# Kernel optimization log

Hardware: AMD Instinct MI355X
Metric: run time of the kernel (lower is better)

## Reference

```python
import jax, jax.numpy as jnp
import numpy as np

N_NODES = 50000
N_EDGES = 640000
D_IN = 128
D_HID = 128


def gcn_conv(x, W, b, src, dst, num_nodes):
    """PyG GCNConv: add self-loops, symmetric normalization, aggregate at target.

    src/dst already include self-loops. x: [N, F_in], W: [F_in, F_out].
    """
    h = x @ W  # [N, F_out] dense transform first (PyG default order)
    ones = jnp.ones(src.shape[0], dtype=h.dtype)
    deg = jax.ops.segment_sum(ones, dst, num_segments=num_nodes)  # in-degree w/ self loops
    dinv = jnp.where(deg > 0, jax.lax.rsqrt(deg), 0.0)
    norm = dinv[src] * dinv[dst]  # [E+N]
    msgs = h[src] * norm[:, None]  # gather + edge-wise scale
    out = jax.ops.segment_sum(msgs, dst, num_segments=num_nodes)  # scatter-add at target
    return out + b


def setup_inputs() -> dict:
    key = jax.random.key(0)
    k1, k2, k3, k4 = jax.random.split(key, 4)
    x = jax.random.normal(k1, (N_NODES, D_IN), dtype=jnp.float32)
    edge_index = jax.random.randint(k2, (2, N_EDGES), 0, N_NODES, dtype=jnp.int64)
    # Glorot-ish init for weights
    W1 = jax.random.normal(k3, (D_IN, D_HID), dtype=jnp.float32) * (1.0 / np.sqrt(D_IN))
    b1 = jnp.zeros((D_HID,), dtype=jnp.float32)
    W2 = jax.random.normal(k4, (D_HID, D_HID), dtype=jnp.float32) * (1.0 / np.sqrt(D_HID))
    b2 = jnp.zeros((D_HID,), dtype=jnp.float32)
    return {"x": x, "edge_index": edge_index, "W1": W1, "b1": b1, "W2": W2, "b2": b2}


def reference(x, edge_index, W1, b1, W2, b2):
    num_nodes = x.shape[0]
    loop = jnp.arange(num_nodes, dtype=edge_index.dtype)
    src = jnp.concatenate([edge_index[0], loop])  # add self-loops once; shared by both convs
    dst = jnp.concatenate([edge_index[1], loop])
    h = jax.nn.relu(gcn_conv(x, W1, b1, src, dst, num_nodes))
    out = gcn_conv(h, W2, b2, src, dst, num_nodes)
    return out
```

## Files before the change

### kernel.cpp

```cpp
#include <hip/hip_runtime.h>

#define NN 50000
#define NE 640000
#define DF 128
#define BM 64
#define BSH 7
#define BWD 128
#define NBKT ((NN + BWD - 1) / BWD)
#define BSTRIDE 4096
#define CPAD 16
#define EPB 8192
#define TPB 512
#define MROWS 50048

typedef __attribute__((ext_vector_type(8))) short short8;
typedef __attribute__((ext_vector_type(4))) float f32x4;

__device__ inline unsigned bf16rne(float f) {
  unsigned u = __float_as_uint(f);
  return (u + 0x7fff + ((u >> 16) & 1)) >> 16;
}
__device__ inline float bflo(unsigned u) { return __uint_as_float(u << 16); }
__device__ inline float bfhi(unsigned u) { return __uint_as_float(u & 0xffff0000u); }
__device__ inline float bfs(unsigned short h) { return __uint_as_float(((unsigned)h) << 16); }


__global__ __launch_bounds__(512) void k_zb(int* __restrict__ gfill) {
  for (int i = threadIdx.x; i < NBKT * CPAD; i += 512) gfill[i] = 0;
}

__global__ __launch_bounds__(512) void k_bscatter(const int* __restrict__ ei, int* __restrict__ gfill,
                                                  unsigned* __restrict__ pairs) {
  __shared__ int cnt[NBKT];
  __shared__ int cur[NBKT];
  __shared__ int gbase[NBKT];
  __shared__ int scan[TPB];
  __shared__ unsigned stage[EPB];
  int t = threadIdx.x;
  int e0 = blockIdx.x * EPB;

  for (int i = t; i < NBKT; i += TPB) cnt[i] = 0;
  __syncthreads();

  unsigned pk[16];
  int bk[16];
#pragma unroll
  for (int i = 0; i < 16; ++i) {
    int e = e0 + i * TPB + t;
    if (e < NE) {
      int s = ei[e], d = ei[NE + e];
      bk[i] = d >> BSH;
      pk[i] = (unsigned)s | ((unsigned)(d & (BWD - 1)) << 16);
      atomicAdd(&cnt[bk[i]], 1);
    } else {
      bk[i] = -1;
    }
  }
  __syncthreads();

  int v = (t < NBKT) ? cnt[t] : 0;
  scan[t] = v;
  __syncthreads();
  for (int d = 1; d < TPB; d <<= 1) {
    int x = (t >= d) ? scan[t - d] : 0;
    __syncthreads();
    scan[t] += x;
    __syncthreads();
  }
  if (t < NBKT) {
    int start = scan[t] - v;
    cnt[t] = start;
    cur[t] = start;
    gbase[t] = (v > 0) ? atomicAdd(&gfill[t * CPAD], v) : 0;
  }
  __syncthreads();

#pragma unroll
  for (int i = 0; i < 16; ++i) {
    if (bk[i] >= 0) {
      int pos = atomicAdd(&cur[bk[i]], 1);
      stage[pos] = pk[i];
    }
  }
  __syncthreads();

  int wv = t >> 6, ln = t & 63;
  for (int b = wv; b < NBKT; b += 8) {
    int start = cnt[b];
    int end = cur[b];
    int gb = gbase[b];
    unsigned* pb = pairs + (size_t)b * BSTRIDE;
    for (int i = start + ln; i < end; i += 64) {
      int go = gb + (i - start);
      if (go < BSTRIDE) pb[go] = stage[i];
    }
  }
}

__global__ __launch_bounds__(512) void k_bscan(const int* __restrict__ gfill, int* __restrict__ boff) {
  __shared__ int s[512];
  int t = threadIdx.x;
  int v = (t < NBKT) ? min(gfill[t * CPAD], BSTRIDE) : 0;
  s[t] = v;
  __syncthreads();
  for (int d = 1; d < 512; d <<= 1) {
    int x = (t >= d) ? s[t - d] : 0;
    __syncthreads();
    s[t] += x;
    __syncthreads();
  }
  if (t < NBKT) boff[t] = s[t] - v;
  if (t == 511) boff[NBKT] = s[511];
}

__global__ __launch_bounds__(256) void k_build(const unsigned* __restrict__ pairs,
                                               const int* __restrict__ boff,
                                               int* __restrict__ off, float* __restrict__ dinv,
                                               unsigned short* __restrict__ ssrc) {
  __shared__ int lcnt[BWD];
  __shared__ int lfill[BWD];
  __shared__ int s[BWD];
  __shared__ unsigned short stage[BSTRIDE];
  int b = blockIdx.x, t = threadIdx.x;
  int e0 = boff[b];
  int n = boff[b + 1] - e0;
  const unsigned* pb = pairs + (size_t)b * BSTRIDE;

  if (t < BWD) lcnt[t] = 0;
  __syncthreads();
  for (int i = t; i < n; i += 256) atomicAdd(&lcnt[pb[i] >> 16], 1);
  __syncthreads();

  int cnt = (t < BWD) ? lcnt[t] : 0;
  if (t < BWD) s[t] = cnt;
  __syncthreads();
  for (int d = 1; d < BWD; d <<= 1) {
    int x = (t >= d && t < BWD) ? s[t - d] : 0;
    __syncthreads();
    if (t < BWD) s[t] += x;
    __syncthreads();
  }
  int node = b * BWD + t;
  if (t < BWD) {
    int ex = s[t] - cnt;
    lfill[t] = ex;
    if (node < NN) {
      off[node] = e0 + ex;
      dinv[node] = rsqrtf((float)(cnt + 1));
    }
    if (node == NN - 1) off[NN] = NE;
  }
  __syncthreads();

  for (int i = t; i < n; i += 256) {
    unsigned p = pb[i];
    int pos = atomicAdd(&lfill[p >> 16], 1);
    stage[pos] = (unsigned short)(p & 0xffffu);
  }
  __syncthreads();
  for (int i = t; i < n; i += 256) ssrc[e0 + i] = stage[i];
}


__global__ __launch_bounds__(256) void k_wpack(const float* __restrict__ W1, const float* __restrict__ W2,
                                               uint4* __restrict__ whf, uint4* __restrict__ wlf) {
  int idx = blockIdx.x * 256 + threadIdx.x;
  if (idx >= 4096) return;
  int m = idx >> 11;
  int r = idx & 2047;
  int ct = r >> 8, kc = (r >> 6) & 3, l = r & 63;
  const float* W = m ? W2 : W1;
  unsigned hi[8], lo[8];
#pragma unroll
  for (int j = 0; j < 8; ++j) {
    int k = kc * 32 + (l >> 4) * 8 + j;
    int c = ct * 16 + (l & 15);
    float w = W[k * DF + c];
    unsigned h = bf16rne(w);
    hi[j] = h;
    lo[j] = bf16rne(w - bflo(h));
  }
  uint4 H, L;
  H.x = hi[0] | (hi[1] << 16); H.y = hi[2] | (hi[3] << 16);
  H.z = hi[4] | (hi[5] << 16); H.w = hi[6] | (hi[7] << 16);
  L.x = lo[0] | (lo[1] << 16); L.y = lo[2] | (lo[3] << 16);
  L.z = lo[4] | (lo[5] << 16); L.w = lo[6] | (lo[7] << 16);
  whf[idx] = H;
  wlf[idx] = L;
}


template <int ABF16>
__global__ __launch_bounds__(256) void k_gemm(const void* __restrict__ Av,
                                              const uint4* __restrict__ whf,
                                              const uint4* __restrict__ wlf,
                                              const float* __restrict__ dinv,
                                              unsigned* __restrict__ C) {
  __shared__ float Ep[4][16][132];
  int t = threadIdx.x, w = t >> 6, l = t & 63;
  int brow = blockIdx.x * BM + w * 16;
  int ra = brow + (l & 15);
  bool inb = ra < NN;

  short8 Ah[4], Al[4];
#pragma unroll
  for (int kc = 0; kc < 4; ++kc) {
    if (ABF16) {
      uint4 u = make_uint4(0, 0, 0, 0);
      if (inb) u = ((const uint4*)Av)[(size_t)ra * 16 + kc * 4 + (l >> 4)];
      Ah[kc] = *(short8*)&u;
      Al[kc] = short8{0, 0, 0, 0, 0, 0, 0, 0};
    } else {
      float f[8] = {0.f, 0.f, 0.f, 0.f, 0.f, 0.f, 0.f, 0.f};
      if (inb) {
        const float* A = (const float*)Av + (size_t)ra * DF + kc * 32 + (l >> 4) * 8;
        float4 p = *(const float4*)A;
        float4 q = *(const float4*)(A + 4);
        f[0] = p.x; f[1] = p.y; f[2] = p.z; f[3] = p.w;
        f[4] = q.x; f[5] = q.y; f[6] = q.z; f[7] = q.w;
      }
      unsigned hh[8], ll[8];
#pragma unroll
      for (int j = 0; j < 8; ++j) {
        hh[j] = bf16rne(f[j]);
        ll[j] = bf16rne(f[j] - bflo(hh[j]));
      }
      uint4 H, L;
      H.x = hh[0] | (hh[1] << 16); H.y = hh[2] | (hh[3] << 16);
      H.z = hh[4] | (hh[5] << 16); H.w = hh[6] | (hh[7] << 16);
      L.x = ll[0] | (ll[1] << 16); L.y = ll[2] | (ll[3] << 16);
      L.z = ll[4] | (ll[5] << 16); L.w = ll[6] | (ll[7] << 16);
      Ah[kc] = *(short8*)&H;
      Al[kc] = *(short8*)&L;
    }
  }

  f32x4 acc[8];
#pragma unroll
  for (int ct = 0; ct < 8; ++ct) acc[ct] = f32x4{0.f, 0.f, 0.f, 0.f};

#pragma unroll
  for (int kc = 0; kc < 4; ++kc) {
#pragma unroll
    for (int ct = 0; ct < 8; ++ct) {
      int fi = (ct * 4 + kc) * 64 + l;
      uint4 wh4 = whf[fi];
      uint4 wl4 = wlf[fi];
      short8 wh = *(short8*)&wh4;
      short8 wl = *(short8*)&wl4;
      acc[ct] = __builtin_amdgcn_mfma_f32_16x16x32_bf16(Ah[kc], wh, acc[ct], 0, 0, 0);
      acc[ct] = __builtin_amdgcn_mfma_f32_16x16x32_bf16(Ah[kc], wl, acc[ct], 0, 0, 0);
      if (!ABF16)
        acc[ct] = __builtin_amdgcn_mfma_f32_16x16x32_bf16(Al[kc], wh, acc[ct], 0, 0, 0);
    }
  }

#pragma unroll
  for (int ct = 0; ct < 8; ++ct) {
#pragma unroll
    for (int reg = 0; reg < 4; ++reg)
      Ep[w][(l >> 4) * 4 + reg][ct * 16 + (l & 15)] = acc[ct][reg];
  }

  int r16 = l >> 2, cc = (l & 3) * 32;
  int R = blockIdx.x * BM + w * 16 + r16;
  float sc = (R < NN) ? dinv[R] : 0.f;
  unsigned ub[16];
#pragma unroll
  for (int i = 0; i < 16; ++i) {
    float f0 = Ep[w][r16][cc + 2 * i] * sc;
    float f1 = Ep[w][r16][cc + 2 * i + 1] * sc;
    ub[i] = bf16rne(f0) | (bf16rne(f1) << 16);
  }
  uint4* co = (uint4*)(C + (size_t)R * 64 + (cc >> 1));
  co[0] = make_uint4(ub[0], ub[1], ub[2], ub[3]);
  co[1] = make_uint4(ub[4], ub[5], ub[6], ub[7]);
  co[2] = make_uint4(ub[8], ub[9], ub[10], ub[11]);
  co[3] = make_uint4(ub[12], ub[13], ub[14], ub[15]);
}


template <int OUTBF16>
__global__ __launch_bounds__(256) void k_agg(const unsigned* __restrict__ h, const float* __restrict__ dinv,
                                             const int* __restrict__ off, const unsigned short* __restrict__ ssrc,
                                             const float* __restrict__ bias, void* __restrict__ out) {
  int gw = (blockIdx.x * 256 + threadIdx.x) >> 6;
  int lane = threadIdx.x & 63;
  if (gw >= NN) return;

  int c = lane & 15;
  int q = lane >> 4;

  float acc[8];
  {
    uint4 u = *((const uint4*)(h + (size_t)gw * 64) + c);
    float m = (q == 0) ? 1.f : 0.f;
    acc[0] = bflo(u.x) * m; acc[1] = bfhi(u.x) * m;
    acc[2] = bflo(u.y) * m; acc[3] = bfhi(u.y) * m;
    acc[4] = bflo(u.z) * m; acc[5] = bfhi(u.z) * m;
    acc[6] = bflo(u.w) * m; acc[7] = bfhi(u.w) * m;
  }

  int e = off[gw], e1 = off[gw + 1];
  for (int e0 = e; e0 < e1; e0 += 8) {
    int ea = e0 + q;
    int eb = e0 + 4 + q;
    int sa = (ea < e1) ? (int)ssrc[ea] : NN;
    int sb = (eb < e1) ? (int)ssrc[eb] : NN;
    uint4 ua = *((const uint4*)(h + (size_t)sa * 64) + c);
    uint4 ub = *((const uint4*)(h + (size_t)sb * 64) + c);
    acc[0] += bflo(ua.x); acc[1] += bfhi(ua.x);
    acc[2] += bflo(ua.y); acc[3] += bfhi(ua.y);
    acc[4] += bflo(ua.z); acc[5] += bfhi(ua.z);
    acc[6] += bflo(ua.w); acc[7] += bfhi(ua.w);
    acc[0] += bflo(ub.x); acc[1] += bfhi(ub.x);
    acc[2] += bflo(ub.y); acc[3] += bfhi(ub.y);
    acc[4] += bflo(ub.z); acc[5] += bfhi(ub.z);
    acc[6] += bflo(ub.w); acc[7] += bfhi(ub.w);
  }

#pragma unroll
  for (int j = 0; j < 8; ++j) {
    acc[j] += __shfl_xor(acc[j], 16);
    acc[j] += __shfl_xor(acc[j], 32);
  }

  if (q < 2) {
    float di = dinv[gw];
    int col0 = c * 8 + q * 4;
    float4 b4 = *(const float4*)(bias + col0);
    float o0 = fmaf(acc[q * 4 + 0], di, b4.x);
    float o1 = fmaf(acc[q * 4 + 1], di, b4.y);
    float o2 = fmaf(acc[q * 4 + 2], di, b4.z);
    float o3 = fmaf(acc[q * 4 + 3], di, b4.w);
    if (OUTBF16) {
      o0 = fmaxf(o0, 0.f); o1 = fmaxf(o1, 0.f);
      o2 = fmaxf(o2, 0.f); o3 = fmaxf(o3, 0.f);
      uint2 p;
      p.x = bf16rne(o0) | (bf16rne(o1) << 16);
      p.y = bf16rne(o2) | (bf16rne(o3) << 16);
      *(uint2*)((unsigned*)out + (size_t)gw * (DF / 2) + c * 4 + q * 2) = p;
    } else {
      float4 o = make_float4(o0, o1, o2, o3);
      *(float4*)((float*)out + (size_t)gw * DF + col0) = o;
    }
  }
}


extern "C" void kernel_launch(void* const* d_in, const int* in_sizes, int n_in,
                              void* d_out, int out_size, void* d_ws, size_t ws_size,
                              hipStream_t stream) {
  const float* x  = (const float*)d_in[0];
  const int*   ei = (const int*)d_in[1];
  const float* W1 = (const float*)d_in[2];
  const float* b1 = (const float*)d_in[3];
  const float* W2 = (const float*)d_in[4];
  const float* b2 = (const float*)d_in[5];
  float* out = (float*)d_out;

  char* ws = (char*)d_ws;
  unsigned* hT    = (unsigned*)ws; ws += (size_t)MROWS * (DF / 2) * 4;
  unsigned* act   = (unsigned*)ws; ws += (size_t)MROWS * (DF / 2) * 4;
  unsigned* pairs = (unsigned*)ws; ws += (size_t)NBKT * BSTRIDE * 4;
  uint4* whf = (uint4*)ws;  ws += (size_t)4096 * 16;
  uint4* wlf = (uint4*)ws;  ws += (size_t)4096 * 16;
  int*   off  = (int*)ws;   ws += (size_t)(NN + 1) * 4;
  int*   gfill= (int*)ws;   ws += (size_t)NBKT * CPAD * 4;
  int*   boff = (int*)ws;   ws += (size_t)(NBKT + 1) * 4;
  float* dinv = (float*)ws; ws += (size_t)NN * 4;
  unsigned short* ssrc = (unsigned short*)ws; ws += ((size_t)NE + 16) * 2;

  const int GGRID = MROWS / BM;

  k_zb<<<1, 512, 0, stream>>>(gfill);
  k_bscatter<<<(NE + EPB - 1) / EPB, TPB, 0, stream>>>(ei, gfill, pairs);
  k_bscan<<<1, 512, 0, stream>>>(gfill, boff);
  k_wpack<<<16, 256, 0, stream>>>(W1, W2, whf, wlf);
  k_build<<<NBKT, 256, 0, stream>>>(pairs, boff, off, dinv, ssrc);

  k_gemm<0><<<GGRID, 256, 0, stream>>>(x, whf, wlf, dinv, hT);
  k_agg<1><<<(NN * 64 + 255) / 256, 256, 0, stream>>>(hT, dinv, off, ssrc, b1, act);
  k_gemm<1><<<GGRID, 256, 0, stream>>>(act, whf + 2048, wlf + 2048, dinv, hT);
  k_agg<0><<<(NN * 64 + 255) / 256, 256, 0, stream>>>(hT, dinv, off, ssrc, b2, out);
}
```

Measured before the change: 138.8 us.

## Fuse graph build with first GEMM and layer-1 aggregation with second GEMM

Cuts the pipeline from nine launches to five. Weight packing and bucket-counter zeroing share one kernel. Edge bucket-scatter and the first dense transform run as disjoint block ranges of a single launch, so they can overlap. The separate bucket scan is folded into the build kernel, where each block reduces the earlier bucket counts itself. The layer-1 aggregation now writes its 64-row tile of activations into shared memory and feeds the second MFMA GEMM in the same kernel, and the dinv[src] scaling moves into the gather instead of the first GEMM epilogue. Buckets are widened to 256 nodes, which halves the bucket count. The costs are serialised aggregation of 16 rows per wave pass inside each fused block, lower occupancy, and redundant prefix sums across build blocks.

```diff
diff --git a/kernel.cpp b/kernel.cpp
--- a/kernel.cpp
+++ b/kernel.cpp
@@ -3,15 +3,15 @@
 #define NN 50000
 #define NE 640000
 #define DF 128
-#define BM 64
-#define BSH 7
-#define BWD 128
-#define NBKT ((NN + BWD - 1) / BWD)
-#define BSTRIDE 4096
+#define BSH 8
+#define BWD 256
+#define NBKT 196
+#define BSTRIDE 8192
 #define CPAD 16
 #define EPB 8192
-#define TPB 512
+#define NSB ((NE + EPB - 1) / EPB)
 #define MROWS 50048
+#define GG 782
 
 typedef __attribute__((ext_vector_type(8))) short short8;
 typedef __attribute__((ext_vector_type(4))) float f32x4;
@@ -22,150 +22,16 @@
 }
 __device__ inline float bflo(unsigned u) { return __uint_as_float(u << 16); }
 __device__ inline float bfhi(unsigned u) { return __uint_as_float(u & 0xffff0000u); }
-__device__ inline float bfs(unsigned short h) { return __uint_as_float(((unsigned)h) << 16); }
-
-
-__global__ __launch_bounds__(512) void k_zb(int* __restrict__ gfill) {
-  for (int i = threadIdx.x; i < NBKT * CPAD; i += 512) gfill[i] = 0;
-}
-
-__global__ __launch_bounds__(512) void k_bscatter(const int* __restrict__ ei, int* __restrict__ gfill,
-                                                  unsigned* __restrict__ pairs) {
-  __shared__ int cnt[NBKT];
-  __shared__ int cur[NBKT];
-  __shared__ int gbase[NBKT];
-  __shared__ int scan[TPB];
-  __shared__ unsigned stage[EPB];
-  int t = threadIdx.x;
-  int e0 = blockIdx.x * EPB;
-
-  for (int i = t; i < NBKT; i += TPB) cnt[i] = 0;
-  __syncthreads();
-
-  unsigned pk[16];
-  int bk[16];
-#pragma unroll
-  for (int i = 0; i < 16; ++i) {
-    int e = e0 + i * TPB + t;
-    if (e < NE) {
-      int s = ei[e], d = ei[NE + e];
-      bk[i] = d >> BSH;
-      pk[i] = (unsigned)s | ((unsigned)(d & (BWD - 1)) << 16);
-      atomicAdd(&cnt[bk[i]], 1);
-    } else {
-      bk[i] = -1;
-    }
-  }
-  __syncthreads();
-
-  int v = (t < NBKT) ? cnt[t] : 0;
-  scan[t] = v;
-  __syncthreads();
-  for (int d = 1; d < TPB; d <<= 1) {
-    int x = (t >= d) ? scan[t - d] : 0;
-    __syncthreads();
-    scan[t] += x;
-    __syncthreads();
-  }
-  if (t < NBKT) {
-    int start = scan[t] - v;
-    cnt[t] = start;
-    cur[t] = start;
-    gbase[t] = (v > 0) ? atomicAdd(&gfill[t * CPAD], v) : 0;
-  }
-  __syncthreads();
-
-#pragma unroll
-  for (int i = 0; i < 16; ++i) {
-    if (bk[i] >= 0) {
-      int pos = atomicAdd(&cur[bk[i]], 1);
-      stage[pos] = pk[i];
-    }
-  }
-  __syncthreads();
-
-  int wv = t >> 6, ln = t & 63;
-  for (int b = wv; b < NBKT; b += 8) {
-    int start = cnt[b];
-    int end = cur[b];
-    int gb = gbase[b];
-    unsigned* pb = pairs + (size_t)b * BSTRIDE;
-    for (int i = start + ln; i < end; i += 64) {
-      int go = gb + (i - start);
-      if (go < BSTRIDE) pb[go] = stage[i];
-    }
-  }
-}
-
-__global__ __launch_bounds__(512) void k_bscan(const int* __restrict__ gfill, int* __restrict__ boff) {
-  __shared__ int s[512];
-  int t = threadIdx.x;
-  int v = (t < NBKT) ? min(gfill[t * CPAD], BSTRIDE) : 0;
-  s[t] = v;
-  __syncthreads();
-  for (int d = 1; d < 512; d <<= 1) {
-    int x = (t >= d) ? s[t - d] : 0;
-    __syncthreads();
-    s[t] += x;
-    __syncthreads();
-  }
-  if (t < NBKT) boff[t] = s[t] - v;
-  if (t == 511) boff[NBKT] = s[511];
-}
-
-__global__ __launch_bounds__(256) void k_build(const unsigned* __restrict__ pairs,
-                                               const int* __restrict__ boff,
-                                               int* __restrict__ off, float* __restrict__ dinv,
-                                               unsigned short* __restrict__ ssrc) {
-  __shared__ int lcnt[BWD];
-  __shared__ int lfill[BWD];
-  __shared__ int s[BWD];
-  __shared__ unsigned short stage[BSTRIDE];
-  int b = blockIdx.x, t = threadIdx.x;
-  int e0 = boff[b];
-  int n = boff[b + 1] - e0;
-  const unsigned* pb = pairs + (size_t)b * BSTRIDE;
-
-  if (t < BWD) lcnt[t] = 0;
-  __syncthreads();
-  for (int i = t; i < n; i += 256) atomicAdd(&lcnt[pb[i] >> 16], 1);
-  __syncthreads();
-
-  int cnt = (t < BWD) ? lcnt[t] : 0;
-  if (t < BWD) s[t] = cnt;
-  __syncthreads();
-  for (int d = 1; d < BWD; d <<= 1) {
-    int x = (t >= d && t < BWD) ? s[t - d] : 0;
-    __syncthreads();
-    if (t < BWD) s[t] += x;
-    __syncthreads();
-  }
-  int node = b * BWD + t;
-  if (t < BWD) {
-    int ex = s[t] - cnt;
-    lfill[t] = ex;
-    if (node < NN) {
-      off[node] = e0 + ex;
-      dinv[node] = rsqrtf((float)(cnt + 1));
-    }
-    if (node == NN - 1) off[NN] = NE;
-  }
-  __syncthreads();
-
-  for (int i = t; i < n; i += 256) {
-    unsigned p = pb[i];
-    int pos = atomicAdd(&lfill[p >> 16], 1);
-    stage[pos] = (unsigned short)(p & 0xffffu);
-  }
-  __syncthreads();
-  for (int i = t; i < n; i += 256) ssrc[e0 + i] = stage[i];
-}
-
-
-__global__ __launch_bounds__(256) void k_wpack(const float* __restrict__ W1, const float* __restrict__ W2,
-                                               uint4* __restrict__ whf, uint4* __restrict__ wlf) {
+
+
+__global__ __launch_bounds__(256) void k_wz(const float* __restrict__ W1, const float* __restrict__ W2,
+                                            uint4* __restrict__ whf, uint4* __restrict__ wlf,
+                                            int* __restrict__ gfill) {
+  if (blockIdx.x == 16) {
+    for (int i = threadIdx.x; i < NBKT * CPAD; i += 256) gfill[i] = 0;
+    return;
+  }
   int idx = blockIdx.x * 256 + threadIdx.x;
-  if (idx >= 4096) return;
   int m = idx >> 11;
   int r = idx & 2047;
   int ct = r >> 8, kc = (r >> 6) & 3, l = r & 63;
@@ -190,34 +56,96 @@
 }
 
 
-template <int ABF16>
-__global__ __launch_bounds__(256) void k_gemm(const void* __restrict__ Av,
-                                              const uint4* __restrict__ whf,
-                                              const uint4* __restrict__ wlf,
-                                              const float* __restrict__ dinv,
-                                              unsigned* __restrict__ C) {
-  __shared__ float Ep[4][16][132];
-  int t = threadIdx.x, w = t >> 6, l = t & 63;
-  int brow = blockIdx.x * BM + w * 16;
-  int ra = brow + (l & 15);
-  bool inb = ra < NN;
-
-  short8 Ah[4], Al[4];
-#pragma unroll
-  for (int kc = 0; kc < 4; ++kc) {
-    if (ABF16) {
-      uint4 u = make_uint4(0, 0, 0, 0);
-      if (inb) u = ((const uint4*)Av)[(size_t)ra * 16 + kc * 4 + (l >> 4)];
-      Ah[kc] = *(short8*)&u;
-      Al[kc] = short8{0, 0, 0, 0, 0, 0, 0, 0};
-    } else {
+struct ScatSh {
+  int cnt[NBKT], cur[NBKT], gbase[NBKT];
+  int scan[256];
+  unsigned stage[EPB];
+};
+struct GemmSh { float Ep[4][16][132]; };
+union SgSh { ScatSh s; GemmSh g; };
+
+__global__ __launch_bounds__(256) void k_sg(const int* __restrict__ ei, int* __restrict__ gfill,
+                                            unsigned* __restrict__ pairs,
+                                            const float* __restrict__ X,
+                                            const uint4* __restrict__ whf, const uint4* __restrict__ wlf,
+                                            unsigned* __restrict__ hA) {
+  __shared__ SgSh sh;
+  int t = threadIdx.x;
+
+  if (blockIdx.x < NSB) {
+    int e0 = blockIdx.x * EPB;
+    for (int i = t; i < NBKT; i += 256) sh.s.cnt[i] = 0;
+    __syncthreads();
+
+    unsigned pk[32];
+    int bk[32];
+#pragma unroll
+    for (int i = 0; i < 32; ++i) {
+      int e = e0 + i * 256 + t;
+      if (e < NE) {
+        int s = ei[e], d = ei[NE + e];
+        bk[i] = d >> BSH;
+        pk[i] = (unsigned)s | ((unsigned)(d & (BWD - 1)) << 16);
+        atomicAdd(&sh.s.cnt[bk[i]], 1);
+      } else {
+        bk[i] = -1;
+      }
+    }
+    __syncthreads();
+
+    int v = (t < NBKT) ? sh.s.cnt[t] : 0;
+    sh.s.scan[t] = v;
+    __syncthreads();
+    for (int d = 1; d < 256; d <<= 1) {
+      int x2 = (t >= d) ? sh.s.scan[t - d] : 0;
+      __syncthreads();
+      sh.s.scan[t] += x2;
+      __syncthreads();
+    }
+    if (t < NBKT) {
+      int start = sh.s.scan[t] - v;
+      sh.s.cnt[t] = start;
+      sh.s.cur[t] = start;
+      sh.s.gbase[t] = (v > 0) ? atomicAdd(&gfill[t * CPAD], v) : 0;
+    }
+    __syncthreads();
+
+#pragma unroll
+    for (int i = 0; i < 32; ++i) {
+      if (bk[i] >= 0) {
+        int pos = atomicAdd(&sh.s.cur[bk[i]], 1);
+        sh.s.stage[pos] = pk[i];
+      }
+    }
+    __syncthreads();
+
+    int wv = t >> 6, ln = t & 63;
+    for (int b = wv; b < NBKT; b += 4) {
+      int start = sh.s.cnt[b];
+      int end = sh.s.cur[b];
+      int gb = sh.s.gbase[b];
+      unsigned* pb = pairs + (size_t)b * BSTRIDE;
+      for (int i = start + ln; i < end; i += 64) {
+        int go = gb + (i - start);
+        if (go < BSTRIDE) pb[go] = sh.s.stage[i];
+      }
+    }
+  } else {
+    int w = t >> 6, l = t & 63;
+    int brow = (blockIdx.x - NSB) * 64 + w * 16;
+    int ra = brow + (l & 15);
+    bool inb = ra < NN;
+
+    short8 Ah[4], Al[4];
+#pragma unroll
+    for (int kc = 0; kc < 4; ++kc) {
       float f[8] = {0.f, 0.f, 0.f, 0.f, 0.f, 0.f, 0.f, 0.f};
       if (inb) {
-        const float* A = (const float*)Av + (size_t)ra * DF + kc * 32 + (l >> 4) * 8;
+        const float* A = X + (size_t)ra * DF + kc * 32 + (l >> 4) * 8;
         float4 p = *(const float4*)A;
-        float4 q = *(const float4*)(A + 4);
+        float4 qq = *(const float4*)(A + 4);
         f[0] = p.x; f[1] = p.y; f[2] = p.z; f[3] = p.w;
-        f[4] = q.x; f[5] = q.y; f[6] = q.z; f[7] = q.w;
+        f[4] = qq.x; f[5] = qq.y; f[6] = qq.z; f[7] = qq.w;
       }
       unsigned hh[8], ll[8];
 #pragma unroll
@@ -233,11 +161,189 @@
       Ah[kc] = *(short8*)&H;
       Al[kc] = *(short8*)&L;
     }
-  }
-
-  f32x4 acc[8];
-#pragma unroll
-  for (int ct = 0; ct < 8; ++ct) acc[ct] = f32x4{0.f, 0.f, 0.f, 0.f};
+
+    f32x4 acc[8];
+#pragma unroll
+    for (int ct = 0; ct < 8; ++ct) acc[ct] = f32x4{0.f, 0.f, 0.f, 0.f};
+
+#pragma unroll
+    for (int kc = 0; kc < 4; ++kc) {
+#pragma unroll
+      for (int ct = 0; ct < 8; ++ct) {
+        int fi = (ct * 4 + kc) * 64 + l;
+        uint4 wh4 = whf[fi];
+        uint4 wl4 = wlf[fi];
+        short8 wh = *(short8*)&wh4;
+        short8 wl = *(short8*)&wl4;
+        acc[ct] = __builtin_amdgcn_mfma_f32_16x16x32_bf16(Ah[kc], wh, acc[ct], 0, 0, 0);
+        acc[ct] = __builtin_amdgcn_mfma_f32_16x16x32_bf16(Ah[kc], wl, acc[ct], 0, 0, 0);
+        acc[ct] = __builtin_amdgcn_mfma_f32_16x16x32_bf16(Al[kc], wh, acc[ct], 0, 0, 0);
+      }
+    }
+
+#pragma unroll
+    for (int ct = 0; ct < 8; ++ct)
+#pragma unroll
+      for (int reg = 0; reg < 4; ++reg)
+        sh.g.Ep[w][(l >> 4) * 4 + reg][ct * 16 + (l & 15)] = acc[ct][reg];
+
+    int r16 = l >> 2, cc = (l & 3) * 32;
+    int R = (blockIdx.x - NSB) * 64 + w * 16 + r16;
+    float sc = (R < NN) ? 1.f : 0.f;
+    unsigned ub[16];
+#pragma unroll
+    for (int i = 0; i < 16; ++i) {
+      float f0 = sh.g.Ep[w][r16][cc + 2 * i] * sc;
+      float f1 = sh.g.Ep[w][r16][cc + 2 * i + 1] * sc;
+      ub[i] = bf16rne(f0) | (bf16rne(f1) << 16);
+    }
+    uint4* co = (uint4*)(hA + (size_t)R * 64 + (cc >> 1));
+    co[0] = make_uint4(ub[0], ub[1], ub[2], ub[3]);
+    co[1] = make_uint4(ub[4], ub[5], ub[6], ub[7]);
+    co[2] = make_uint4(ub[8], ub[9], ub[10], ub[11]);
+    co[3] = make_uint4(ub[12], ub[13], ub[14], ub[15]);
+  }
+}
+
+
+__global__ __launch_bounds__(256) void k_build(const unsigned* __restrict__ pairs,
+                                               const int* __restrict__ gfill,
+                                               int* __restrict__ off, float* __restrict__ dinv,
+                                               unsigned short* __restrict__ ssrc) {
+  __shared__ int lcnt[BWD];
+  __shared__ int lfill[BWD];
+  __shared__ int s[BWD];
+  __shared__ int red[256];
+  __shared__ unsigned short stage[BSTRIDE];
+  int b = blockIdx.x, t = threadIdx.x;
+
+  int part = 0;
+  for (int j = t; j < b; j += 256) part += min(gfill[j * CPAD], BSTRIDE);
+  red[t] = part;
+  __syncthreads();
+  for (int d = 128; d > 0; d >>= 1) {
+    if (t < d) red[t] += red[t + d];
+    __syncthreads();
+  }
+  int e0 = red[0];
+  int n = min(gfill[b * CPAD], BSTRIDE);
+  const unsigned* pb = pairs + (size_t)b * BSTRIDE;
+
+  lcnt[t] = 0;
+  __syncthreads();
+  for (int i = t; i < n; i += 256) atomicAdd(&lcnt[pb[i] >> 16], 1);
+  __syncthreads();
+
+  int cnt = lcnt[t];
+  s[t] = cnt;
+  __syncthreads();
+  for (int d = 1; d < 256; d <<= 1) {
+    int x = (t >= d) ? s[t - d] : 0;
+    __syncthreads();
+    s[t] += x;
+    __syncthreads();
+  }
+  int node = b * BWD + t;
+  int ex = s[t] - cnt;
+  lfill[t] = ex;
+  if (node < NN) {
+    off[node] = e0 + ex;
+    dinv[node] = rsqrtf((float)(cnt + 1));
+  }
+  if (node == NN - 1) off[NN] = NE;
+  __syncthreads();
+
+  for (int i = t; i < n; i += 256) {
+    unsigned p = pb[i];
+    int pos = atomicAdd(&lfill[p >> 16], 1);
+    stage[pos] = (unsigned short)(p & 0xffffu);
+  }
+  __syncthreads();
+  for (int i = t; i < n; i += 256) ssrc[e0 + i] = stage[i];
+}
+
+
+__global__ __launch_bounds__(256) void k_aggemm(const unsigned* __restrict__ hA,
+                                                const float* __restrict__ dinv,
+                                                const int* __restrict__ off,
+                                                const unsigned short* __restrict__ ssrc,
+                                                const float* __restrict__ b1,
+                                                const uint4* __restrict__ whf,
+                                                const uint4* __restrict__ wlf,
+                                                unsigned* __restrict__ hB) {
+  __shared__ unsigned actS[64][68];
+  __shared__ float Ep[4][16][132];
+  int t = threadIdx.x, w = t >> 6, l = t & 63;
+  int brow = blockIdx.x * 64;
+  int c = l & 15, q = l >> 4;
+
+  for (int it = 0; it < 16; ++it) {
+    int r = it * 4 + w;
+    int g = brow + r;
+    if (g < NN) {
+      float di = dinv[g];
+      float acc[8];
+      uint4 u0 = *((const uint4*)(hA + (size_t)g * 64) + c);
+      float m = (q == 0) ? di : 0.f;
+      acc[0] = bflo(u0.x) * m; acc[1] = bfhi(u0.x) * m;
+      acc[2] = bflo(u0.y) * m; acc[3] = bfhi(u0.y) * m;
+      acc[4] = bflo(u0.z) * m; acc[5] = bfhi(u0.z) * m;
+      acc[6] = bflo(u0.w) * m; acc[7] = bfhi(u0.w) * m;
+
+      int e = off[g], e1 = off[g + 1];
+      for (int eb0 = e; eb0 < e1; eb0 += 8) {
+        int ea = eb0 + q, eb = eb0 + 4 + q;
+        int sa = (ea < e1) ? (int)ssrc[ea] : NN;
+        int sb = (eb < e1) ? (int)ssrc[eb] : NN;
+        float wa = (ea < e1) ? dinv[sa] : 0.f;
+        float wb = (eb < e1) ? dinv[sb] : 0.f;
+        uint4 ua = *((const uint4*)(hA + (size_t)sa * 64) + c);
+        uint4 ub = *((const uint4*)(hA + (size_t)sb * 64) + c);
+        acc[0] = fmaf(bflo(ua.x), wa, acc[0]); acc[1] = fmaf(bfhi(ua.x), wa, acc[1]);
+        acc[2] = fmaf(bflo(ua.y), wa, acc[2]); acc[3] = fmaf(bfhi(ua.y), wa, acc[3]);
+        acc[4] = fmaf(bflo(ua.z), wa, acc[4]); acc[5] = fmaf(bfhi(ua.z), wa, acc[5]);
+        acc[6] = fmaf(bflo(ua.w), wa, acc[6]); acc[7] = fmaf(bfhi(ua.w), wa, acc[7]);
+        acc[0] = fmaf(bflo(ub.x), wb, acc[0]); acc[1] = fmaf(bfhi(ub.x), wb, acc[1]);
+        acc[2] = fmaf(bflo(ub.y), wb, acc[2]); acc[3] = fmaf(bfhi(ub.y), wb, acc[3]);
+        acc[4] = fmaf(bflo(ub.z), wb, acc[4]); acc[5] = fmaf(bfhi(ub.z), wb, acc[5]);
+        acc[6] = fmaf(bflo(ub.w), wb, acc[6]); acc[7] = fmaf(bfhi(ub.w), wb, acc[7]);
+      }
+
+#pragma unroll
+      for (int j = 0; j < 8; ++j) {
+        acc[j] += __shfl_xor(acc[j], 16);
+        acc[j] += __shfl_xor(acc[j], 32);
+      }
+
+      if (q < 2) {
+        int col0 = c * 8 + q * 4;
+        float4 b4 = *(const float4*)(b1 + col0);
+        float o0 = fmaxf(fmaf(acc[q * 4 + 0], di, b4.x), 0.f);
+        float o1 = fmaxf(fmaf(acc[q * 4 + 1], di, b4.y), 0.f);
+        float o2 = fmaxf(fmaf(acc[q * 4 + 2], di, b4.z), 0.f);
+        float o3 = fmaxf(fmaf(acc[q * 4 + 3], di, b4.w), 0.f);
+        uint2 p;
+        p.x = bf16rne(o0) | (bf16rne(o1) << 16);
+        p.y = bf16rne(o2) | (bf16rne(o3) << 16);
+        *(uint2*)&actS[r][c * 4 + q * 2] = p;
+      }
+    } else {
+      if (q < 2) *(uint2*)&actS[r][c * 4 + q * 2] = make_uint2(0u, 0u);
+    }
+  }
+  __syncthreads();
+
+  short8 Ah[4];
+  int lr = w * 16 + (l & 15);
+#pragma unroll
+  for (int kc = 0; kc < 4; ++kc) {
+    uint4 u = *(const uint4*)&actS[lr][(kc * 4 + (l >> 4)) * 4];
+    Ah[kc] = *(short8*)&u;
+  }
+
+  f32x4 acc2[8];
+#pragma unroll
+  for (int ct = 0; ct < 8; ++ct) acc2[ct] = f32x4{0.f, 0.f, 0.f, 0.f};
 
 #pragma unroll
   for (int kc = 0; kc < 4; ++kc) {
@@ -248,22 +354,19 @@
       uint4 wl4 = wlf[fi];
       short8 wh = *(short8*)&wh4;
       short8 wl = *(short8*)&wl4;
-      acc[ct] = __builtin_amdgcn_mfma_f32_16x16x32_bf16(Ah[kc], wh, acc[ct], 0, 0, 0);
-      acc[ct] = __builtin_amdgcn_mfma_f32_16x16x32_bf16(Ah[kc], wl, acc[ct], 0, 0, 0);
-      if (!ABF16)
-        acc[ct] = __builtin_amdgcn_mfma_f32_16x16x32_bf16(Al[kc], wh, acc[ct], 0, 0, 0);
-    }
-  }
-
-#pragma unroll
-  for (int ct = 0; ct < 8; ++ct) {
+      acc2[ct] = __builtin_amdgcn_mfma_f32_16x16x32_bf16(Ah[kc], wh, acc2[ct], 0, 0, 0);
+      acc2[ct] = __builtin_amdgcn_mfma_f32_16x16x32_bf16(Ah[kc], wl, acc2[ct], 0, 0, 0);
+    }
+  }
+
+#pragma unroll
+  for (int ct = 0; ct < 8; ++ct)
 #pragma unroll
     for (int reg = 0; reg < 4; ++reg)
-      Ep[w][(l >> 4) * 4 + reg][ct * 16 + (l & 15)] = acc[ct][reg];
-  }
+      Ep[w][(l >> 4) * 4 + reg][ct * 16 + (l & 15)] = acc2[ct][reg];
 
   int r16 = l >> 2, cc = (l & 3) * 32;
-  int R = blockIdx.x * BM + w * 16 + r16;
+  int R = brow + w * 16 + r16;
   float sc = (R < NN) ? dinv[R] : 0.f;
   unsigned ub[16];
 #pragma unroll
@@ -272,7 +375,7 @@
     float f1 = Ep[w][r16][cc + 2 * i + 1] * sc;
     ub[i] = bf16rne(f0) | (bf16rne(f1) << 16);
   }
-  uint4* co = (uint4*)(C + (size_t)R * 64 + (cc >> 1));
+  uint4* co = (uint4*)(hB + (size_t)R * 64 + (cc >> 1));
   co[0] = make_uint4(ub[0], ub[1], ub[2], ub[3]);
   co[1] = make_uint4(ub[4], ub[5], ub[6], ub[7]);
   co[2] = make_uint4(ub[8], ub[9], ub[10], ub[11]);
@@ -280,10 +383,9 @@
 }
 
 
-template <int OUTBF16>
-__global__ __launch_bounds__(256) void k_agg(const unsigned* __restrict__ h, const float* __restrict__ dinv,
-                                             const int* __restrict__ off, const unsigned short* __restrict__ ssrc,
-                                             const float* __restrict__ bias, void* __restrict__ out) {
+__global__ __launch_bounds__(256) void k_agg2(const unsigned* __restrict__ h, const float* __restrict__ dinv,
+                                              const int* __restrict__ off, const unsigned short* __restrict__ ssrc,
+                                              const float* __restrict__ bias, float* __restrict__ out) {
   int gw = (blockIdx.x * 256 + threadIdx.x) >> 6;
   int lane = threadIdx.x & 63;
   if (gw >= NN) return;
@@ -329,21 +431,12 @@
     float di = dinv[gw];
     int col0 = c * 8 + q * 4;
     float4 b4 = *(const float4*)(bias + col0);
-    float o0 = fmaf(acc[q * 4 + 0], di, b4.x);
-    float o1 = fmaf(acc[q * 4 + 1], di, b4.y);
-    float o2 = fmaf(acc[q * 4 + 2], di, b4.z);
-    float o3 = fmaf(acc[q * 4 + 3], di, b4.w);
-    if (OUTBF16) {
-      o0 = fmaxf(o0, 0.f); o1 = fmaxf(o1, 0.f);
-      o2 = fmaxf(o2, 0.f); o3 = fmaxf(o3, 0.f);
-      uint2 p;
-      p.x = bf16rne(o0) | (bf16rne(o1) << 16);
-      p.y = bf16rne(o2) | (bf16rne(o3) << 16);
-      *(uint2*)((unsigned*)out + (size_t)gw * (DF / 2) + c * 4 + q * 2) = p;
-    } else {
-      float4 o = make_float4(o0, o1, o2, o3);
-      *(float4*)((float*)out + (size_t)gw * DF + col0) = o;
-    }
+    float4 o;
+    o.x = fmaf(acc[q * 4 + 0], di, b4.x);
+    o.y = fmaf(acc[q * 4 + 1], di, b4.y);
+    o.z = fmaf(acc[q * 4 + 2], di, b4.z);
+    o.w = fmaf(acc[q * 4 + 3], di, b4.w);
+    *(float4*)(out + (size_t)gw * DF + col0) = o;
   }
 }
 
@@ -360,27 +453,19 @@
   float* out = (float*)d_out;
 
   char* ws = (char*)d_ws;
-  unsigned* hT    = (unsigned*)ws; ws += (size_t)MROWS * (DF / 2) * 4;
-  unsigned* act   = (unsigned*)ws; ws += (size_t)MROWS * (DF / 2) * 4;
+  unsigned* hA    = (unsigned*)ws; ws += (size_t)MROWS * 64 * 4;
+  unsigned* hB    = (unsigned*)ws; ws += (size_t)MROWS * 64 * 4;
   unsigned* pairs = (unsigned*)ws; ws += (size_t)NBKT * BSTRIDE * 4;
   uint4* whf = (uint4*)ws;  ws += (size_t)4096 * 16;
   uint4* wlf = (uint4*)ws;  ws += (size_t)4096 * 16;
   int*   off  = (int*)ws;   ws += (size_t)(NN + 1) * 4;
   int*   gfill= (int*)ws;   ws += (size_t)NBKT * CPAD * 4;
-  int*   boff = (int*)ws;   ws += (size_t)(NBKT + 1) * 4;
   float* dinv = (float*)ws; ws += (size_t)NN * 4;
   unsigned short* ssrc = (unsigned short*)ws; ws += ((size_t)NE + 16) * 2;
 
-  const int GGRID = MROWS / BM;
-
-  k_zb<<<1, 512, 0, stream>>>(gfill);
-  k_bscatter<<<(NE + EPB - 1) / EPB, TPB, 0, stream>>>(ei, gfill, pairs);
-  k_bscan<<<1, 512, 0, stream>>>(gfill, boff);
-  k_wpack<<<16, 256, 0, stream>>>(W1, W2, whf, wlf);
-  k_build<<<NBKT, 256, 0, stream>>>(pairs, boff, off, dinv, ssrc);
-
-  k_gemm<0><<<GGRID, 256, 0, stream>>>(x, whf, wlf, dinv, hT);
-  k_agg<1><<<(NN * 64 + 255) / 256, 256, 0, stream>>>(hT, dinv, off, ssrc, b1, act);
-  k_gemm<1><<<GGRID, 256, 0, stream>>>(act, whf + 2048, wlf + 2048, dinv, hT);
-  k_agg<0><<<(NN * 64 + 255) / 256, 256, 0, stream>>>(hT, dinv, off, ssrc, b2, out);
-}
+  k_wz<<<17, 256, 0, stream>>>(W1, W2, whf, wlf, gfill);
+  k_sg<<<NSB + GG, 256, 0, stream>>>(ei, gfill, pairs, x, whf, wlf, hA);
+  k_build<<<NBKT, 256, 0, stream>>>(pairs, gfill, off, dinv, ssrc);
+  k_aggemm<<<GG, 256, 0, stream>>>(hA, dinv, off, ssrc, b1, whf + 2048, wlf + 2048, hB);
+  k_agg2<<<(NN * 64 + 255) / 256, 256, 0, stream>>>(hB, dinv, off, ssrc, b2, out);
+}
```

Measured after the change: 169.2 us. +21.9%, slower.
